# Kernel optimization log

Hardware: AMD Instinct MI355X
Metric: run time of the kernel (lower is better)

The kernel has to match this reference:

```python
import jax, jax.numpy as jnp
import numpy as np

B, V, N = 256, 50, 32
D, H, L, CS, NN, OUT = 128, 384, 12, 10, 10000, 128
ND = N * D          # per-visit input dim
G = 4 * H + 2 * L   # gate projection width
CH = H // L         # chunk size
HS = H // 6         # scale bottleneck


def setup_inputs() -> dict:
    key = jax.random.key(0)
    ks = jax.random.split(key, 20)
    s = 0.02
    embed = jax.random.normal(ks[0], (NN + 1, D), jnp.float32) * s
    embed = embed.at[0].set(0.0)  # padding_idx=0
    inp = {
        'node_ids': jax.random.randint(ks[1], (B, V, N), 0, NN + 1),
        'edge_idx': jax.random.randint(ks[2], (2, 128), 0, NN),
        'edge_attr': jax.random.normal(ks[3], (128,), jnp.float32),
        'time': jax.random.uniform(ks[4], (B, V), jnp.float32),
        'visit_order': jax.random.randint(ks[5], (B, V), 0, V),
        'attn_mask': jnp.ones((B, V), jnp.bool_),
        'embed': embed,
        'kernel_w': jax.random.normal(ks[6], (G, ND + 1), jnp.float32) * s,
        'kernel_b': jnp.zeros((G,), jnp.float32),
        'rec_w': jax.random.normal(ks[7], (G, H + 1), jnp.float32) * s,
        'rec_b': jnp.zeros((G,), jnp.float32),
        'scale_w': jax.random.normal(ks[8], (HS, H), jnp.float32) * s,
        'scale_b': jnp.zeros((HS,), jnp.float32),
        'rescale_w': jax.random.normal(ks[9], (H, HS), jnp.float32) * s,
        'rescale_b': jnp.zeros((H,), jnp.float32),
        'conv_w': jax.random.normal(ks[10], (H, H, CS), jnp.float32) * s,
        'conv_b': jnp.zeros((H,), jnp.float32),
        'out_w': jax.random.normal(ks[11], (OUT, V * H), jnp.float32) * s,
        'out_b': jnp.zeros((OUT,), jnp.float32),
    }
    return inp


def _cumax_l2r(x):
    return jnp.cumsum(jax.nn.softmax(x, -1), -1)


def _cumax_r2l(x):
    return jnp.flip(jnp.cumsum(jax.nn.softmax(jnp.flip(x, -1), -1), -1), -1)


def _forward(node_ids, time, embed, kernel_w, kernel_b, rec_w, rec_b,
             scale_w, scale_b, rescale_w, rescale_b, conv_w, conv_b, out_w, out_b):
    x = embed[node_ids].reshape(B, V, ND)  # gather per-visit code embeddings

    def step(carry, xs):
        c, h, tmp_h, tmp_dis = carry
        x_t, t_t = xs
        iv = t_t[:, None]
        xo = (jnp.concatenate([x_t, iv], -1) @ kernel_w.T + kernel_b
              + jnp.concatenate([h, iv], -1) @ rec_w.T + rec_b)
        fm = _cumax_l2r(xo[:, :L])              # [B,L] master forget
        im = _cumax_r2l(xo[:, L:2 * L])         # [B,L] master input
        g = xo[:, 2 * L:].reshape(B, 4 * L, CH)
        f = jax.nn.sigmoid(g[:, :L])
        i_ = jax.nn.sigmoid(g[:, L:2 * L])
        o = jax.nn.sigmoid(g[:, 2 * L:3 * L])
        cin = jnp.tanh(g[:, 3 * L:])
        cl = c.reshape(B, L, CH)
        fmE, imE = fm[:, :, None], im[:, :, None]
        ov = fmE * imE
        cnew = ov * (f * cl + i_ * cin) + (fmE - ov) * cl + (imE - ov) * cin
        hnew = (o * jnp.tanh(cnew)).reshape(B, H)
        cnew = cnew.reshape(B, H)
        dist = 1.0 - jnp.mean(fm, -1)           # [B]
        tmp_h = jnp.concatenate([tmp_h[1:], hnew[None]], 0)    # [CS,B,H]
        tmp_dis = jnp.concatenate([tmp_dis[1:], dist[None]], 0)  # [CS,B]
        ld = jax.nn.softmax(jnp.cumsum(tmp_dis.T, 1), 1)       # [B,CS]
        lh = tmp_h.transpose(1, 2, 0) * ld[:, None, :]         # [B,H,CS]
        theme = jax.nn.sigmoid(
            jnp.maximum(jnp.mean(lh, -1) @ scale_w.T + scale_b, 0.0)
            @ rescale_w.T + rescale_b)
        conv = jnp.einsum('bhk,ohk->bo', lh, conv_w) + conv_b  # valid conv, len 1
        local = theme * conv
        return (cnew, hnew, tmp_h, tmp_dis), (local, hnew, dist)

    c0 = jnp.zeros((B, H), jnp.float32)
    h0 = jnp.zeros((B, H), jnp.float32)
    tmp_h0 = jnp.zeros((CS, B, H), jnp.float32)
    tmp_dis0 = jnp.zeros((CS, B), jnp.float32)
    xs = (x.transpose(1, 0, 2), time.T)
    _, (hs, ohs, dists) = jax.lax.scan(step, (c0, h0, tmp_h0, tmp_dis0), xs)
    rnn = hs.transpose(1, 0, 2) + ohs.transpose(1, 0, 2)       # [B,V,H]
    out = rnn.reshape(B, V * H) @ out_w.T + out_b
    return out, dists  # dists: [V,B]


def reference(node_ids, edge_idx, edge_attr, time, visit_order, attn_mask,
              embed, kernel_w, kernel_b, rec_w, rec_b, scale_w, scale_b,
              rescale_w, rescale_b, conv_w, conv_b, out_w, out_b):
    # edge_idx / edge_attr / visit_order / attn_mask are unused by StageNet.forward
    return _forward(node_ids, time, embed, kernel_w, kernel_b, rec_w, rec_b,
                    scale_w, scale_b, rescale_w, rescale_b, conv_w, conv_b,
                    out_w, out_b)
```

## Files before the change

kernel.cpp:

```cpp
#include <hip/hip_runtime.h>
#include <math.h>

typedef _Float16 f16;
typedef _Float16 f16x8 __attribute__((ext_vector_type(8)));
typedef float f32x4 __attribute__((ext_vector_type(4)));
typedef unsigned int u32;
typedef u32 u32x4 __attribute__((ext_vector_type(4)));

#define DEV static __device__ __forceinline__

DEV float sigm(float x)  { return 1.0f / (1.0f + __expf(-x)); }
DEV float tanhfast(float x) { return 2.0f / (1.0f + __expf(-2.0f * x)) - 1.0f; }

DEV void gld16(const void* g, void* l) {
  __builtin_amdgcn_global_load_lds((const __attribute__((address_space(1))) void*)g,
                                   (__attribute__((address_space(3))) void*)l, 16, 0, 0);
}

DEV void gbar(int* bar, int nblk) {
  __syncthreads();
  if (threadIdx.x == 0) {
    int* cnt = bar;
    int* gen = bar + 16;
    int g = __hip_atomic_load(gen, __ATOMIC_RELAXED, __HIP_MEMORY_SCOPE_AGENT);
    int a = __hip_atomic_fetch_add(cnt, 1, __ATOMIC_RELEASE, __HIP_MEMORY_SCOPE_AGENT);
    if (a == nblk - 1) {
      __hip_atomic_store(cnt, 0, __ATOMIC_RELAXED, __HIP_MEMORY_SCOPE_AGENT);
      __hip_atomic_store(gen, g + 1, __ATOMIC_RELEASE, __HIP_MEMORY_SCOPE_AGENT);
    } else {
      while (__hip_atomic_load(gen, __ATOMIC_RELAXED, __HIP_MEMORY_SCOPE_AGENT) == g)
        __builtin_amdgcn_s_sleep(1);
    }
    (void)__hip_atomic_load(gen, __ATOMIC_ACQUIRE, __HIP_MEMORY_SCOPE_AGENT);
  }
  __syncthreads();
}

#define GP 1664
#define KH 3840
#define KO 19200
#define ZSPLIT 40
#define NGRP 16
#define NMEM 12
#define NBLK 192
#define XOLS 164
#define RECUR_LDS (122880 + 10496 + 1024)

static constexpr size_t OFF_OPART = 0;
static constexpr size_t OFF_ZB    = 104857600 - 262144;
static constexpr size_t OFF_WK    = 104857600;
static constexpr size_t OFF_XK    = OFF_WK + 13631488;
static constexpr size_t OFF_MLH   = OFF_XK;
static constexpr size_t OFF_S1    = OFF_XK + 9830400;
static constexpr size_t OFF_TH    = OFF_XK + 13107200;
static constexpr size_t OFF_CV    = OFF_XK + 32768000;
static constexpr size_t OFF_SWP   = OFF_XK + 72089600;
static constexpr size_t OFF_RWP2  = OFF_XK + 72187904;
static constexpr size_t OFF_SBP   = OFF_XK + 72286208;
static constexpr size_t OFF_RW    = OFF_XK + 85196800;
static constexpr size_t OFF_SV    = OFF_RW + 1474560;
static constexpr size_t OFF_BAR   = OFF_SV + 8192;
static constexpr size_t OFF_BIASC = OFF_BAR + 32768;
static constexpr size_t OFF_HALL  = OFF_BIASC + 8192;
static constexpr size_t OFF_LD    = OFF_HALL + 9830400;
static constexpr size_t OFF_WC2   = OFF_LD + 512000;
static constexpr size_t OFF_RNN   = OFF_WC2 + 2949120;
static constexpr size_t OFF_OUTW  = OFF_RNN + 9830400;
static constexpr size_t OFF_EH    = OFF_OUTW + 4915200;


__global__ __launch_bounds__(256) void k_prep_wk(const float* __restrict__ kw,
                                                 const float* __restrict__ kb,
                                                 const float* __restrict__ rb,
                                                 f16* __restrict__ Wk,
                                                 float* __restrict__ biasc) {
  long i = (long)blockIdx.x * 256 + threadIdx.x;
  if (i < 1664L * 4096 / 8) {
    long base = i * 8;
    int nn = (int)(base >> 12);
    int k  = (int)(base & 4095);
    f16x8 o;
    if (nn < 1560) {
      const float* s = kw + (long)nn * 4097 + k;
#pragma unroll
      for (int e = 0; e < 8; ++e) o[e] = (f16)s[e];
    } else {
#pragma unroll
      for (int e = 0; e < 8; ++e) o[e] = (f16)0.0f;
    }
    *(f16x8*)(Wk + base) = o;
  }
  if (i < 1664) biasc[i] = (i < 1560) ? (kb[i] + rb[i]) : 0.0f;
}

__global__ __launch_bounds__(512) void k_prep_misc(const float* __restrict__ rw,
                                                   const float* __restrict__ kw,
                                                   const float* __restrict__ sw,
                                                   const float* __restrict__ sb,
                                                   const float* __restrict__ rw2,
                                                   const float* __restrict__ cw,
                                                   const float* __restrict__ ow,
                                                   const float* __restrict__ embed,
                                                   f16* __restrict__ RWp,
                                                   float* __restrict__ Sv,
                                                   int* __restrict__ bar,
                                                   f16* __restrict__ swp,
                                                   float* __restrict__ sbp,
                                                   f16* __restrict__ rwp2,
                                                   f16* __restrict__ Wc2,
                                                   f16* __restrict__ outw,
                                                   f16* __restrict__ Eh) {
  const int blk = blockIdx.x, tid = threadIdx.x;
  if (blk < 180) {
    int i = blk * 512 + tid;
    if (i < 92160) {
      int p = i / 7680;
      int rem = i - p * 7680;
      int tau = rem / 768;
      int r2 = rem - tau * 768;
      int f = r2 >> 6;
      int l = r2 & 63;
      int lc = tau * 16 + (l & 15);
      int n;
      if (lc < 24) n = lc;
      else if (lc < 32) n = -1;
      else { int run = (lc - 32) >> 5; n = 24 + (run * 12 + p) * 32 + ((lc - 32) & 31); }
      int k = f * 32 + ((l >> 4) << 3);
      f16x8 o;
      if (n >= 0) {
        const float* s = rw + (long)n * 385 + k;
#pragma unroll
        for (int e = 0; e < 8; ++e) o[e] = (f16)s[e];
      } else {
#pragma unroll
        for (int e = 0; e < 8; ++e) o[e] = (f16)0.0f;
      }
      *(f16x8*)(RWp + (long)i * 8) = o;
    }
    if (i < 1664)
      Sv[i] = (i < 1560) ? (rw[(long)i * 385 + 384] + kw[(long)i * 4097 + 4096]) : 0.0f;
    if (i < 8192) bar[i] = 0;
  } else if (blk < 276) {
    int i = (blk - 180) * 512 + tid;
    if (i < 128 * 384) {
      int o = i / 384, k = i - o * 384;
      swp[i] = (f16)((o < 64) ? sw[o * 384 + k] : 0.0f);
      int o2 = i >> 7, k2 = i & 127;
      rwp2[i] = (f16)((k2 < 64) ? rw2[o2 * 64 + k2] : 0.0f);
    }
    if (i < 128) sbp[i] = (i < 64) ? sb[i] : 0.0f;
  } else if (blk < 636) {
    int i = (blk - 276) * 512 + tid;
    if (i < 184320) {
      int base = i * 8;
      int o = base / 3840;
      int c = base - o * 3840;
      int j = c / 384;
      int h = c - j * 384;
      f16x8 v;
#pragma unroll
      for (int e = 0; e < 8; ++e) v[e] = (f16)cw[((long)o * 384 + h + e) * 10 + j];
      *(f16x8*)(Wc2 + base) = v;
    }
  } else if (blk < 1236) {
    long i = (long)(blk - 636) * 512 + tid;
    if (i < 307200) {
      long base = i * 8;
      float4 a = *(const float4*)(ow + base);
      float4 b2 = *(const float4*)(ow + base + 4);
      f16x8 v;
      v[0] = (f16)a.x;  v[1] = (f16)a.y;  v[2] = (f16)a.z;  v[3] = (f16)a.w;
      v[4] = (f16)b2.x; v[5] = (f16)b2.y; v[6] = (f16)b2.z; v[7] = (f16)b2.w;
      *(f16x8*)(outw + base) = v;
    }
  } else {
    long i = (long)(blk - 1236) * 512 + tid;
    if (i < 160016) {
      long base = i * 8;
      float4 a = *(const float4*)(embed + base);
      float4 b2 = *(const float4*)(embed + base + 4);
      f16x8 v;
      v[0] = (f16)a.x;  v[1] = (f16)a.y;  v[2] = (f16)a.z;  v[3] = (f16)a.w;
      v[4] = (f16)b2.x; v[5] = (f16)b2.y; v[6] = (f16)b2.z; v[7] = (f16)b2.w;
      *(f16x8*)(Eh + base) = v;
    }
  }
}

__global__ __launch_bounds__(256, 2) void k_gemm_emb(const int* __restrict__ ids,
                                                     const f16* __restrict__ Eh,
                                                     const f16* __restrict__ W,
                                                     f16* __restrict__ C,
                                                     const float* __restrict__ bias) {
  __shared__ __align__(16) f16 As0[256 * 32];
  __shared__ __align__(16) f16 As1[256 * 32];
  __shared__ __align__(16) f16 Bs0[128 * 32];
  __shared__ __align__(16) f16 Bs1[128 * 32];
  const int tid = threadIdx.x;
  const int W0  = blockIdx.y * 50 + blockIdx.x;
  const int xcd = W0 & 7, idx = W0 >> 3;
  const int nw  = (xcd < 2) ? (xcd * 82 + idx) : (164 + (xcd - 2) * 81 + idx);
  const int bx  = nw % 50, by = nw / 50;
  const long rowA0 = (long)bx * 256;
  const long rowB0 = (long)by * 128;
  const int w = tid >> 6, lane = tid & 63;
  const int q = lane >> 4, r16 = lane & 15;
  f32x4 acc[4][8] = {};
  const int srow = tid >> 2;
  const int scol = (tid & 3) * 8;
  const int* idr0 = ids + (rowA0 + srow) * 32;
  const int* idr1 = idr0 + 64 * 32;
  const int* idr2 = idr0 + 128 * 32;
  const int* idr3 = idr0 + 192 * 32;
  const f16* gB0 = W + (rowB0 + srow) * 4096L + scol;
  const f16* gB1 = gB0 + 64L * 4096;
  f16* lA0 = As0 + tid * 8;
  f16* lA1 = As1 + tid * 8;
  f16* lB0 = Bs0 + tid * 8;
  f16* lB1 = Bs1 + tid * 8;
  int cur0 = idr0[0], cur1 = idr1[0], cur2 = idr2[0], cur3 = idr3[0];
  for (int n = 0; n < 32; ++n) {
    int nx0 = 0, nx1 = 0, nx2 = 0, nx3 = 0;
    if (n < 31) { nx0 = idr0[n + 1]; nx1 = idr1[n + 1]; nx2 = idr2[n + 1]; nx3 = idr3[n + 1]; }
#pragma unroll
    for (int kk = 0; kk < 2; ++kk) {
      const int k0 = n * 128 + kk * 64;
      const int d = kk * 64 + scol;
      __syncthreads();
      gld16(Eh + (size_t)cur0 * 128 + d,      lA0);
      gld16(Eh + (size_t)cur1 * 128 + d,      lA0 + 2048);
      gld16(Eh + (size_t)cur2 * 128 + d,      lA0 + 4096);
      gld16(Eh + (size_t)cur3 * 128 + d,      lA0 + 6144);
      gld16(Eh + (size_t)cur0 * 128 + d + 32, lA1);
      gld16(Eh + (size_t)cur1 * 128 + d + 32, lA1 + 2048);
      gld16(Eh + (size_t)cur2 * 128 + d + 32, lA1 + 4096);
      gld16(Eh + (size_t)cur3 * 128 + d + 32, lA1 + 6144);
      gld16(gB0 + k0,      lB0);
      gld16(gB1 + k0,      lB0 + 2048);
      gld16(gB0 + k0 + 32, lB1);
      gld16(gB1 + k0 + 32, lB1 + 2048);
      __syncthreads();
      f16x8 af[4], bf[8];
#pragma unroll
      for (int i = 0; i < 4; i++)
        af[i] = *(const f16x8*)&As0[(w * 64 + i * 16 + r16) * 32 + q * 8];
#pragma unroll
      for (int j = 0; j < 8; j++)
        bf[j] = *(const f16x8*)&Bs0[(j * 16 + r16) * 32 + q * 8];
#pragma unroll
      for (int i = 0; i < 4; i++)
#pragma unroll
        for (int j = 0; j < 8; j++)
          acc[i][j] = __builtin_amdgcn_mfma_f32_16x16x32_f16(af[i], bf[j], acc[i][j], 0, 0, 0);
#pragma unroll
      for (int i = 0; i < 4; i++)
        af[i] = *(const f16x8*)&As1[(w * 64 + i * 16 + r16) * 32 + q * 8];
#pragma unroll
      for (int j = 0; j < 8; j++)
        bf[j] = *(const f16x8*)&Bs1[(j * 16 + r16) * 32 + q * 8];
#pragma unroll
      for (int i = 0; i < 4; i++)
#pragma unroll
        for (int j = 0; j < 8; j++)
          acc[i][j] = __builtin_amdgcn_mfma_f32_16x16x32_f16(af[i], bf[j], acc[i][j], 0, 0, 0);
    }
    cur0 = nx0; cur1 = nx1; cur2 = nx2; cur3 = nx3;
  }
#pragma unroll
  for (int i = 0; i < 4; i++)
#pragma unroll
    for (int j = 0; j < 8; j++) {
      long row = rowA0 + w * 64 + i * 16 + q * 4;
      long col = rowB0 + j * 16 + r16;
      float bv = bias[col];
#pragma unroll
      for (int r = 0; r < 4; r++)
        C[(row + r) * (long)GP + col] = (f16)(acc[i][j][r] + bv);
    }
}

__global__ __launch_bounds__(256) void k_gemm_conv(const float* __restrict__ ld,
                                                   const f16* __restrict__ h_all,
                                                   const f16* __restrict__ W,
                                                   float* __restrict__ C) {
  __shared__ __align__(16) f16 As[128 * 32];
  __shared__ __align__(16) f16 Bs[128 * 32];
  const int tid = threadIdx.x;
  const long rowA0 = (long)blockIdx.x * 128;
  const long rowB0 = (long)blockIdx.y * 128;
  const int ks = blockIdx.z * 1920;
  const long zoff = (long)blockIdx.z * (12800L * 384);
  const int w = tid >> 6, lane = tid & 63;
  const int q = lane >> 4, r16 = lane & 15;
  const int wr = w >> 1, wc = w & 1;
  f32x4 acc[4][4] = {};
  const int srow = tid >> 2;
  const int scol = (tid & 3) * 8;
  const int row0 = (int)rowA0 + srow, row1 = row0 + 64;
  const int b0r = row0 / 50, t0r = row0 - b0r * 50;
  const int b1r = row1 / 50, t1r = row1 - b1r * 50;
  const f16* gB0 = W + (rowB0 + srow) * (long)KH + ks + scol;
  const f16* gB1 = gB0 + 64L * KH;
  f16* lB = Bs + tid * 8;
  for (int k0 = 0; k0 < 1920; k0 += 32) {
    const int col0 = ks + k0;
    const int j = col0 / 384;
    const int hh = col0 - j * 384 + scol;
    const int s0 = t0r - 9 + j, s1 = t1r - 9 + j;
    __syncthreads();
    gld16(gB0 + k0, lB);
    gld16(gB1 + k0, lB + 2048);
    f16x8 a0v = {}, a1v = {};
    if (s0 >= 0) {
      const float lv = ld[row0 * 10 + j];
      f16x8 hv = *(const f16x8*)(h_all + ((size_t)s0 * 256 + b0r) * 384 + hh);
#pragma unroll
      for (int e = 0; e < 8; ++e) a0v[e] = (f16)((float)hv[e] * lv);
    }
    if (s1 >= 0) {
      const float lv = ld[row1 * 10 + j];
      f16x8 hv = *(const f16x8*)(h_all + ((size_t)s1 * 256 + b1r) * 384 + hh);
#pragma unroll
      for (int e = 0; e < 8; ++e) a1v[e] = (f16)((float)hv[e] * lv);
    }
    *(f16x8*)&As[srow * 32 + scol] = a0v;
    *(f16x8*)&As[(srow + 64) * 32 + scol] = a1v;
    __syncthreads();
    f16x8 af[4], bfr[4];
#pragma unroll
    for (int i = 0; i < 4; i++) {
      af[i]  = *(const f16x8*)&As[(wr * 64 + i * 16 + r16) * 32 + q * 8];
      bfr[i] = *(const f16x8*)&Bs[(wc * 64 + i * 16 + r16) * 32 + q * 8];
    }
#pragma unroll
    for (int i = 0; i < 4; i++)
#pragma unroll
      for (int j2 = 0; j2 < 4; j2++)
        acc[i][j2] = __builtin_amdgcn_mfma_f32_16x16x32_f16(af[i], bfr[j2], acc[i][j2], 0, 0, 0);
  }
#pragma unroll
  for (int i = 0; i < 4; i++)
#pragma unroll
    for (int j2 = 0; j2 < 4; j2++) {
      long row = rowA0 + wr * 64 + i * 16 + q * 4;
      long col = rowB0 + wc * 64 + j2 * 16 + r16;
#pragma unroll
      for (int r = 0; r < 4; r++)
        C[(row + r) * 384L + col + zoff] = acc[i][j2][r];
    }
}

__global__ __launch_bounds__(256) void k_gemm_bt(const f16* __restrict__ A,
                                                 const f16* __restrict__ W,
                                                 void* __restrict__ Cv,
                                                 const float* __restrict__ bias,
                                                 int N, int K, int kLen, int act) {
  __shared__ __align__(16) f16 As[128 * 32];
  __shared__ __align__(16) f16 Bs[128 * 32];
  const int tid = threadIdx.x;
  const long rowA0 = (long)blockIdx.x * 128;
  const long rowB0 = (long)blockIdx.y * 128;
  const long ks = (long)blockIdx.z * kLen;
  const long zoff = (long)blockIdx.z * ((long)gridDim.x * 128 * N);
  const int w = tid >> 6, lane = tid & 63;
  const int q = lane >> 4, r16 = lane & 15;
  const int wr = w >> 1, wc = w & 1;
  f32x4 acc[4][4] = {};
  const int srow = tid >> 2;
  const int scol = (tid & 3) * 8;
  const f16* gA0 = A + (rowA0 + srow) * (long)K + ks + scol;
  const f16* gA1 = gA0 + 64L * K;
  const f16* gB0 = W + (rowB0 + srow) * (long)K + ks + scol;
  const f16* gB1 = gB0 + 64L * K;
  f16* lA = As + tid * 8;
  f16* lB = Bs + tid * 8;
  for (int k0 = 0; k0 < kLen; k0 += 32) {
    __syncthreads();
    gld16(gA0 + k0, lA);
    gld16(gA1 + k0, lA + 2048);
    gld16(gB0 + k0, lB);
    gld16(gB1 + k0, lB + 2048);
    __syncthreads();
    f16x8 af[4], bfr[4];
#pragma unroll
    for (int i = 0; i < 4; i++) {
      af[i]  = *(const f16x8*)&As[(wr * 64 + i * 16 + r16) * 32 + q * 8];
      bfr[i] = *(const f16x8*)&Bs[(wc * 64 + i * 16 + r16) * 32 + q * 8];
    }
#pragma unroll
    for (int i = 0; i < 4; i++)
#pragma unroll
      for (int j = 0; j < 4; j++)
        acc[i][j] = __builtin_amdgcn_mfma_f32_16x16x32_f16(af[i], bfr[j], acc[i][j], 0, 0, 0);
  }
#pragma unroll
  for (int i = 0; i < 4; i++)
#pragma unroll
    for (int j = 0; j < 4; j++) {
      long row = rowA0 + wr * 64 + i * 16 + q * 4;
      long col = rowB0 + wc * 64 + j * 16 + r16;
      float bv = bias ? bias[col] : 0.0f;
#pragma unroll
      for (int r = 0; r < 4; r++) {
        float v = acc[i][j][r] + bv;
        long off = (row + r) * (long)N + col + zoff;
        if (act == 0)      ((float*)Cv)[off] = v;
        else if (act == 1) ((f16*)Cv)[off]   = (f16)v;
        else if (act == 2) ((f16*)Cv)[off]   = (f16)fmaxf(v, 0.0f);
        else               ((float*)Cv)[off] = sigm(v);
      }
    }
}

__global__ __launch_bounds__(640)
void k_recur_coop(const f16* __restrict__ XKh,
                  const f16* __restrict__ RWp,
                  const float* __restrict__ Sv,
                  const float* __restrict__ timep,
                  f16* __restrict__ zbuf,
                  f16* __restrict__ hall,
                  float* __restrict__ dists,
                  int* __restrict__ bar) {
  extern __shared__ char smem[];
  f16*   Wl  = (f16*)smem;
  float* xol = (float*)(smem + 122880);
  f16*   hl  = (f16*)(smem + 122880 + 10496);
  const int tid = threadIdx.x;
  const int g = blockIdx.x / NMEM;
  const int m = blockIdx.x - g * NMEM;
  const int b0 = g * 16;
  int* gflags = bar + g * 256;
  int* ibar   = bar + 4096 + g * 32;
  const int w = tid >> 6, lane = tid & 63;
  const int q = lane >> 4, r16 = lane & 15;
  {
    const f16* src = RWp + (size_t)m * 61440;
    for (int i = tid; i < 7680; i += 640)
      *(f16x8*)(Wl + (size_t)i * 8) = *(const f16x8*)(src + (size_t)i * 8);
  }
  int ncol = -1; float Svc = 0.0f;
  if (w < 10) {
    const int lc = w * 16 + r16;
    if (lc < 24) ncol = lc;
    else if (lc >= 32) { int run = (lc - 32) >> 5; ncol = 24 + (run * 12 + m) * 32 + ((lc - 32) & 31); }
    if (ncol >= 0) Svc = Sv[ncol];
  }
  {
    f16x8 z = {};
    for (int i = m * 640 + tid; i < 768; i += NMEM * 640)
      *(f16x8*)(zbuf + (size_t)b0 * 384 + (size_t)i * 8) = z;
  }
  gbar(ibar, NMEM);

  const int ch = tid & 31, bloc = tid >> 5;
  float creg = 0.0f;
  f16 xkc[4] = {};
  if (w < 10 && ncol >= 0) {
#pragma unroll
    for (int r = 0; r < 4; ++r)
      xkc[r] = XKh[((long)(b0 + q * 4 + r) * 50) * GP + ncol];
  }

  for (int t = 0; t < 50; ++t) {
    const f16* hprev = (t == 0) ? zbuf : (hall + (size_t)(t - 1) * 98304);
    f16 xkn[4] = {};
    if (w < 10) {
      f16x8 af[12];
      const f16* ab = hprev + (size_t)(b0 + r16) * 384 + q * 8;
#pragma unroll
      for (int f = 0; f < 12; ++f) af[f] = *(const f16x8*)(ab + f * 32);
      if (t < 49 && ncol >= 0) {
#pragma unroll
        for (int r = 0; r < 4; ++r)
          xkn[r] = XKh[((long)(b0 + q * 4 + r) * 50 + (t + 1)) * GP + ncol];
      }
      float tv4[4];
#pragma unroll
      for (int r = 0; r < 4; ++r) tv4[r] = timep[(b0 + q * 4 + r) * 50 + t];
      const f16* bp = Wl + (size_t)w * 6144 + lane * 8;
      f32x4 a0 = {};
#pragma unroll
      for (int f = 0; f < 12; ++f)
        a0 = __builtin_amdgcn_mfma_f32_16x16x32_f16(af[f], *(const f16x8*)(bp + f * 512), a0, 0, 0, 0);
      const int lc = w * 16 + r16;
#pragma unroll
      for (int r = 0; r < 4; ++r)
        xol[(q * 4 + r) * XOLS + lc] = a0[r] + (float)xkc[r] + tv4[r] * Svc;
    }
    __syncthreads();
    if (bloc < 16) {
      const int gb = b0 + bloc;
      const float* xr = xol + bloc * XOLS;
      float e1[12], e2[12], mx1 = -1e30f, mx2 = -1e30f;
#pragma unroll
      for (int l = 0; l < 12; ++l) {
        e1[l] = xr[l];      mx1 = fmaxf(mx1, e1[l]);
        e2[l] = xr[12 + l]; mx2 = fmaxf(mx2, e2[l]);
      }
      float s1 = 0.0f, s2 = 0.0f;
#pragma unroll
      for (int l = 0; l < 12; ++l) {
        e1[l] = __expf(e1[l] - mx1); s1 += e1[l];
        e2[l] = __expf(e2[l] - mx2); s2 += e2[l];
      }
      float cum1 = 0.0f;
      for (int l = 0; l <= m; ++l) cum1 += e1[l];
      const float fmv = cum1 / s1;
      float cum2 = 0.0f;
      for (int l = 11; l >= m; --l) cum2 += e2[l];
      const float imv = cum2 / s2;
      if (m == 0 && ch == 0) {
        float ds = 0.0f;
#pragma unroll
        for (int l = 0; l < 12; ++l) ds += (float)(12 - l) * e1[l];
        dists[t * 256 + gb] = 1.0f - ds / (12.0f * s1);
      }
      const float fv = sigm(xr[32 + ch]);
      const float iv = sigm(xr[64 + ch]);
      const float og = sigm(xr[96 + ch]);
      const float ci = tanhfast(xr[128 + ch]);
      const float ov = fmv * imv;
      const float cn = ov * (fv * creg + iv * ci) + (fmv - ov) * creg + (imv - ov) * ci;
      creg = cn;
      const float hv = og * tanhfast(cn);
      hl[tid] = (f16)hv;
    }
    __syncthreads();
    if (w == 0) {
      f32x4 d = *(const f32x4*)(hl + lane * 8);
      f16* dst = hall + ((size_t)t * 256 + b0 + (lane >> 2)) * 384 + m * 32 + (lane & 3) * 8;
      asm volatile("global_store_dwordx4 %0, %1, off sc0 sc1\n\t"
                   "s_waitcnt vmcnt(0)"
                   :: "v"(dst), "v"(d) : "memory");
      if (lane == 0) {
        int* fp = gflags + m * 16;
        int fv2 = t + 1;
        asm volatile("global_store_dword %0, %1, off sc0 sc1"
                     :: "v"(fp), "v"(fv2) : "memory");
      }
    }
    if (w == 1 && lane < NMEM) {
      while (__hip_atomic_load(gflags + lane * 16, __ATOMIC_RELAXED, __HIP_MEMORY_SCOPE_AGENT) < t + 1)
        __builtin_amdgcn_s_sleep(1);
    }
    __syncthreads();
    asm volatile("" ::: "memory");
#pragma unroll
    for (int r = 0; r < 4; ++r) xkc[r] = xkn[r];
  }
}

__global__ __launch_bounds__(256) void k_ld(const float* __restrict__ dists,
                                            float* __restrict__ ld) {
  int i = blockIdx.x * 256 + threadIdx.x;
  if (i >= 12800) return;
  int b = i / 50, t = i - b * 50;
  float v[10];
  float cum = 0.0f, mx = -1e30f;
#pragma unroll
  for (int j = 0; j < 10; j++) {
    int s = t - 9 + j;
    float d = (s >= 0) ? dists[s * 256 + b] : 0.0f;
    cum += d; v[j] = cum; mx = fmaxf(mx, cum);
  }
  float sum = 0.0f;
#pragma unroll
  for (int j = 0; j < 10; j++) { v[j] = __expf(v[j] - mx); sum += v[j]; }
  float inv = 1.0f / sum;
#pragma unroll
  for (int j = 0; j < 10; j++) ld[i * 10 + j] = v[j] * inv;
}

__global__ __launch_bounds__(256) void k_mlh(const float* __restrict__ ld,
                                             const f16* __restrict__ h_all,
                                             f16* __restrict__ mlh) {
  int idx = blockIdx.x * 256 + threadIdx.x;
  if (idx >= 614400) return;
  int row = idx / 48, hc = (idx - row * 48) * 8;
  int b = row / 50, t = row - b * 50;
  float acc[8] = {};
#pragma unroll
  for (int j = 0; j < 10; j++) {
    int s = t - 9 + j;
    if (s >= 0) {
      float lv = ld[row * 10 + j];
      f16x8 hv = *(const f16x8*)(h_all + ((size_t)s * 256 + b) * 384 + hc);
#pragma unroll
      for (int e = 0; e < 8; ++e) acc[e] += lv * (float)hv[e];
    }
  }
  f16x8 o;
#pragma unroll
  for (int e = 0; e < 8; ++e) o[e] = (f16)(acc[e] * 0.1f);
  *(f16x8*)(mlh + (size_t)row * 384 + hc) = o;
}

__global__ __launch_bounds__(256) void k_rnn(const float* __restrict__ theme,
                                             const float* __restrict__ convp,
                                             const float* __restrict__ cb,
                                             const f16* __restrict__ h_all,
                                             f16* __restrict__ rnn) {
  int idx = blockIdx.x * 256 + threadIdx.x;
  if (idx >= 614400) return;
  int row = idx / 48, hc = (idx - row * 48) * 8;
  int b = row / 50, t = row - b * 50;
  size_t base = (size_t)row * 384 + hc;
  float4 c0 = *(const float4*)(convp + base);
  float4 c1 = *(const float4*)(convp + base + 4);
  float4 d0 = *(const float4*)(convp + 4915200 + base);
  float4 d1 = *(const float4*)(convp + 4915200 + base + 4);
  float4 t0 = *(const float4*)(theme + base);
  float4 t1 = *(const float4*)(theme + base + 4);
  f16x8 hv = *(const f16x8*)(h_all + ((size_t)t * 256 + b) * 384 + hc);
  f16x8 o;
  o[0] = (f16)(t0.x * (c0.x + d0.x + cb[hc + 0]) + (float)hv[0]);
  o[1] = (f16)(t0.y * (c0.y + d0.y + cb[hc + 1]) + (float)hv[1]);
  o[2] = (f16)(t0.z * (c0.z + d0.z + cb[hc + 2]) + (float)hv[2]);
  o[3] = (f16)(t0.w * (c0.w + d0.w + cb[hc + 3]) + (float)hv[3]);
  o[4] = (f16)(t1.x * (c1.x + d1.x + cb[hc + 4]) + (float)hv[4]);
  o[5] = (f16)(t1.y * (c1.y + d1.y + cb[hc + 5]) + (float)hv[5]);
  o[6] = (f16)(t1.z * (c1.z + d1.z + cb[hc + 6]) + (float)hv[6]);
  o[7] = (f16)(t1.w * (c1.w + d1.w + cb[hc + 7]) + (float)hv[7]);
  *(f16x8*)(rnn + base) = o;
}

__global__ __launch_bounds__(256) void k_red(const float* __restrict__ part,
                                             const float* __restrict__ ob,
                                             float* __restrict__ out) {
  int i = blockIdx.x * 256 + threadIdx.x;
  float s = 0.0f;
#pragma unroll
  for (int z = 0; z < ZSPLIT; z++) s += part[z * 32768 + i];
  out[i] = s + ob[i & 127];
}

extern "C" void kernel_launch(void* const* d_in, const int* in_sizes, int n_in,
                              void* d_out, int out_size, void* d_ws, size_t ws_size,
                              hipStream_t stream) {
  (void)in_sizes; (void)n_in; (void)out_size; (void)ws_size;
  const int*   node_ids  = (const int*)  d_in[0];
  const float* timep     = (const float*)d_in[3];
  const float* embed     = (const float*)d_in[6];
  const float* kernel_w  = (const float*)d_in[7];
  const float* kernel_b  = (const float*)d_in[8];
  const float* rec_w     = (const float*)d_in[9];
  const float* rec_b     = (const float*)d_in[10];
  const float* scale_w   = (const float*)d_in[11];
  const float* scale_b   = (const float*)d_in[12];
  const float* rescale_w = (const float*)d_in[13];
  const float* rescale_b = (const float*)d_in[14];
  const float* conv_w    = (const float*)d_in[15];
  const float* conv_b    = (const float*)d_in[16];
  const float* out_w     = (const float*)d_in[17];
  const float* out_b     = (const float*)d_in[18];

  char* ws = (char*)d_ws;
  float* opart   = (float*)(ws + OFF_OPART);
  f16*   zbuf    = (f16*)  (ws + OFF_ZB);
  f16*   Wk      = (f16*)  (ws + OFF_WK);
  f16*   XKh     = (f16*)  (ws + OFF_XK);
  f16*   mlh_h   = (f16*)  (ws + OFF_MLH);
  f16*   s1h     = (f16*)  (ws + OFF_S1);
  float* theme   = (float*)(ws + OFF_TH);
  float* convbuf = (float*)(ws + OFF_CV);
  f16*   swp     = (f16*)  (ws + OFF_SWP);
  f16*   rwp2    = (f16*)  (ws + OFF_RWP2);
  float* sbp     = (float*)(ws + OFF_SBP);
  f16*   RWp     = (f16*)  (ws + OFF_RW);
  float* Sv      = (float*)(ws + OFF_SV);
  int*   bar     = (int*)  (ws + OFF_BAR);
  float* biasc   = (float*)(ws + OFF_BIASC);
  f16*   h_all   = (f16*)  (ws + OFF_HALL);
  float* ldbuf   = (float*)(ws + OFF_LD);
  f16*   Wc2     = (f16*)  (ws + OFF_WC2);
  f16*   rnn     = (f16*)  (ws + OFF_RNN);
  f16*   outw    = (f16*)  (ws + OFF_OUTW);
  f16*   Eh      = (f16*)  (ws + OFF_EH);

  float* outp  = (float*)d_out;
  float* dists = outp + 256 * 128;

  k_prep_wk  <<<3332, 256, 0, stream>>>(kernel_w, kernel_b, rec_b, Wk, biasc);
  k_prep_misc<<<1549, 512, 0, stream>>>(rec_w, kernel_w, scale_w, scale_b, rescale_w,
                                        conv_w, out_w, embed,
                                        RWp, Sv, bar, swp, sbp, rwp2, Wc2, outw, Eh);
  k_gemm_emb<<<dim3(50, 13), 256, 0, stream>>>(node_ids, Eh, Wk, XKh, biasc);
  {
    hipFuncSetAttribute((const void*)k_recur_coop,
                        hipFuncAttributeMaxDynamicSharedMemorySize, RECUR_LDS);
    void* cargs[] = {(void*)&XKh, (void*)&RWp, (void*)&Sv, (void*)&timep,
                     (void*)&zbuf, (void*)&h_all, (void*)&dists, (void*)&bar};
    hipLaunchCooperativeKernel((void*)k_recur_coop, dim3(NBLK), dim3(640),
                               cargs, RECUR_LDS, stream);
  }
  k_ld  <<<50,   256, 0, stream>>>(dists, ldbuf);
  k_mlh <<<2400, 256, 0, stream>>>(ldbuf, h_all, mlh_h);
  k_gemm_bt<<<dim3(100, 1), 256, 0, stream>>>(mlh_h, swp, s1h, sbp, 128, 384, 384, 2);
  k_gemm_bt<<<dim3(100, 3), 256, 0, stream>>>(s1h, rwp2, theme, rescale_b, 384, 128, 128, 3);
  k_gemm_conv<<<dim3(100, 3, 2), 256, 0, stream>>>(ldbuf, h_all, Wc2, convbuf);
  k_rnn <<<2400, 256, 0, stream>>>(theme, convbuf, conv_b, h_all, rnn);
  k_gemm_bt<<<dim3(2, 1, ZSPLIT), 256, 0, stream>>>(rnn, outw, opart, nullptr, 128, KO, KO / ZSPLIT, 0);
  k_red<<<128, 256, 0, stream>>>(opart, out_b, outp);
}
```

Before: 893.0 us.

## Double-buffer gathered GEMM tiles to overlap global loads with MFMA

Restructures the embedding-gather GEMM main loop into a software pipeline over 128 K-steps of 32. The next step's A (gathered embedding rows) and B tiles are issued into the alternate LDS buffer while MFMAs run on the current buffer, with one barrier per step instead of two. The aim is to hide global-load latency behind compute. The cost is finer-grained steps with more barriers per unit of work, and it depends on the async LDS loads being waited on correctly at the barrier.

```diff
diff --git a/kernel.cpp b/kernel.cpp
--- a/kernel.cpp
+++ b/kernel.cpp
@@ -214,57 +214,57 @@
   const int* idr3 = idr0 + 192 * 32;
   const f16* gB0 = W + (rowB0 + srow) * 4096L + scol;
   const f16* gB1 = gB0 + 64L * 4096;
-  f16* lA0 = As0 + tid * 8;
-  f16* lA1 = As1 + tid * 8;
-  f16* lB0 = Bs0 + tid * 8;
-  f16* lB1 = Bs1 + tid * 8;
   int cur0 = idr0[0], cur1 = idr1[0], cur2 = idr2[0], cur3 = idr3[0];
-  for (int n = 0; n < 32; ++n) {
-    int nx0 = 0, nx1 = 0, nx2 = 0, nx3 = 0;
-    if (n < 31) { nx0 = idr0[n + 1]; nx1 = idr1[n + 1]; nx2 = idr2[n + 1]; nx3 = idr3[n + 1]; }
-#pragma unroll
-    for (int kk = 0; kk < 2; ++kk) {
-      const int k0 = n * 128 + kk * 64;
-      const int d = kk * 64 + scol;
-      __syncthreads();
-      gld16(Eh + (size_t)cur0 * 128 + d,      lA0);
-      gld16(Eh + (size_t)cur1 * 128 + d,      lA0 + 2048);
-      gld16(Eh + (size_t)cur2 * 128 + d,      lA0 + 4096);
-      gld16(Eh + (size_t)cur3 * 128 + d,      lA0 + 6144);
-      gld16(Eh + (size_t)cur0 * 128 + d + 32, lA1);
-      gld16(Eh + (size_t)cur1 * 128 + d + 32, lA1 + 2048);
-      gld16(Eh + (size_t)cur2 * 128 + d + 32, lA1 + 4096);
-      gld16(Eh + (size_t)cur3 * 128 + d + 32, lA1 + 6144);
-      gld16(gB0 + k0,      lB0);
-      gld16(gB1 + k0,      lB0 + 2048);
-      gld16(gB0 + k0 + 32, lB1);
-      gld16(gB1 + k0 + 32, lB1 + 2048);
-      __syncthreads();
+  int nx0 = idr0[1], nx1 = idr1[1], nx2 = idr2[1], nx3 = idr3[1];
+
+  {
+    gld16(Eh + (size_t)cur0 * 128 + scol, As0 + tid * 8);
+    gld16(Eh + (size_t)cur1 * 128 + scol, As0 + tid * 8 + 2048);
+    gld16(Eh + (size_t)cur2 * 128 + scol, As0 + tid * 8 + 4096);
+    gld16(Eh + (size_t)cur3 * 128 + scol, As0 + tid * 8 + 6144);
+    gld16(gB0, Bs0 + tid * 8);
+    gld16(gB1, Bs0 + tid * 8 + 2048);
+  }
+  __syncthreads();
+
+#pragma unroll 2
+  for (int s = 0; s < 128; ++s) {
+    if (s < 127) {
+      const int sn = s + 1;
+      if ((sn & 3) == 0) {
+        cur0 = nx0; cur1 = nx1; cur2 = nx2; cur3 = nx3;
+        const int gg = (sn >> 2) + 1;
+        if (gg < 32) { nx0 = idr0[gg]; nx1 = idr1[gg]; nx2 = idr2[gg]; nx3 = idr3[gg]; }
+      }
+      const int n = sn >> 2, kk = sn & 3;
+      const int d = kk * 32 + scol;
+      const int k0 = n * 128 + kk * 32;
+      f16* lA = ((sn & 1) ? As1 : As0) + tid * 8;
+      f16* lB = ((sn & 1) ? Bs1 : Bs0) + tid * 8;
+      gld16(Eh + (size_t)cur0 * 128 + d, lA);
+      gld16(Eh + (size_t)cur1 * 128 + d, lA + 2048);
+      gld16(Eh + (size_t)cur2 * 128 + d, lA + 4096);
+      gld16(Eh + (size_t)cur3 * 128 + d, lA + 6144);
+      gld16(gB0 + k0, lB);
+      gld16(gB1 + k0, lB + 2048);
+    }
+    {
+      const f16* Ab = (s & 1) ? As1 : As0;
+      const f16* Bb = (s & 1) ? Bs1 : Bs0;
       f16x8 af[4], bf[8];
 #pragma unroll
       for (int i = 0; i < 4; i++)
-        af[i] = *(const f16x8*)&As0[(w * 64 + i * 16 + r16) * 32 + q * 8];
+        af[i] = *(const f16x8*)&Ab[(w * 64 + i * 16 + r16) * 32 + q * 8];
 #pragma unroll
       for (int j = 0; j < 8; j++)
-        bf[j] = *(const f16x8*)&Bs0[(j * 16 + r16) * 32 + q * 8];
+        bf[j] = *(const f16x8*)&Bb[(j * 16 + r16) * 32 + q * 8];
 #pragma unroll
       for (int i = 0; i < 4; i++)
 #pragma unroll
         for (int j = 0; j < 8; j++)
           acc[i][j] = __builtin_amdgcn_mfma_f32_16x16x32_f16(af[i], bf[j], acc[i][j], 0, 0, 0);
-#pragma unroll
-      for (int i = 0; i < 4; i++)
-        af[i] = *(const f16x8*)&As1[(w * 64 + i * 16 + r16) * 32 + q * 8];
-#pragma unroll
-      for (int j = 0; j < 8; j++)
-        bf[j] = *(const f16x8*)&Bs1[(j * 16 + r16) * 32 + q * 8];
-#pragma unroll
-      for (int i = 0; i < 4; i++)
-#pragma unroll
-        for (int j = 0; j < 8; j++)
-          acc[i][j] = __builtin_amdgcn_mfma_f32_16x16x32_f16(af[i], bf[j], acc[i][j], 0, 0, 0);
-    }
-    cur0 = nx0; cur1 = nx1; cur2 = nx2; cur3 = nx3;
+    }
+    __syncthreads();
   }
 #pragma unroll
   for (int i = 0; i < 4; i++)
```

Result: slower. 924.8 us (+3.6%).

## Fuse rnn epilogue into conv GEMM and drop split-K partial buffer

Applied to the files above, without the earlier changes.

The conv GEMM now covers the full K range (no split-K over two z slices) with 64-row tiles, and applies the conv bias, theme multiply and h residual directly in its epilogue to write the f16 rnn output. The separate k_rnn kernel and the fp32 conv partial buffers are removed. This saves a launch and the write and re-read of two fp32 12800x384 partial arrays plus the theme read pass. In exchange each block runs a loop twice as long with smaller tiles and lower MFMA reuse, and the epilogue does scattered scalar loads and stores.

```diff
diff --git a/kernel.cpp b/kernel.cpp
--- a/kernel.cpp
+++ b/kernel.cpp
@@ -282,72 +282,63 @@
 __global__ __launch_bounds__(256) void k_gemm_conv(const float* __restrict__ ld,
                                                    const f16* __restrict__ h_all,
                                                    const f16* __restrict__ W,
-                                                   float* __restrict__ C) {
-  __shared__ __align__(16) f16 As[128 * 32];
+                                                   const float* __restrict__ theme,
+                                                   const float* __restrict__ cb,
+                                                   f16* __restrict__ rnn) {
+  __shared__ __align__(16) f16 As[64 * 32];
   __shared__ __align__(16) f16 Bs[128 * 32];
   const int tid = threadIdx.x;
-  const long rowA0 = (long)blockIdx.x * 128;
-  const long rowB0 = (long)blockIdx.y * 128;
-  const int ks = blockIdx.z * 1920;
-  const long zoff = (long)blockIdx.z * (12800L * 384);
+  const int rowA0 = blockIdx.x * 64;
+  const int rowB0 = blockIdx.y * 128;
   const int w = tid >> 6, lane = tid & 63;
   const int q = lane >> 4, r16 = lane & 15;
-  const int wr = w >> 1, wc = w & 1;
-  f32x4 acc[4][4] = {};
+  f32x4 acc[8] = {};
   const int srow = tid >> 2;
   const int scol = (tid & 3) * 8;
-  const int row0 = (int)rowA0 + srow, row1 = row0 + 64;
+  const int row0 = rowA0 + srow;
   const int b0r = row0 / 50, t0r = row0 - b0r * 50;
-  const int b1r = row1 / 50, t1r = row1 - b1r * 50;
-  const f16* gB0 = W + (rowB0 + srow) * (long)KH + ks + scol;
+  const f16* gB0 = W + (rowB0 + srow) * (long)KH + scol;
   const f16* gB1 = gB0 + 64L * KH;
   f16* lB = Bs + tid * 8;
-  for (int k0 = 0; k0 < 1920; k0 += 32) {
-    const int col0 = ks + k0;
-    const int j = col0 / 384;
-    const int hh = col0 - j * 384 + scol;
-    const int s0 = t0r - 9 + j, s1 = t1r - 9 + j;
+  for (int k0 = 0; k0 < 3840; k0 += 32) {
+    const int j = k0 / 384;
+    const int hh = k0 - j * 384 + scol;
+    const int s0 = t0r - 9 + j;
     __syncthreads();
     gld16(gB0 + k0, lB);
     gld16(gB1 + k0, lB + 2048);
-    f16x8 a0v = {}, a1v = {};
+    f16x8 a0v = {};
     if (s0 >= 0) {
       const float lv = ld[row0 * 10 + j];
       f16x8 hv = *(const f16x8*)(h_all + ((size_t)s0 * 256 + b0r) * 384 + hh);
 #pragma unroll
       for (int e = 0; e < 8; ++e) a0v[e] = (f16)((float)hv[e] * lv);
     }
-    if (s1 >= 0) {
-      const float lv = ld[row1 * 10 + j];
-      f16x8 hv = *(const f16x8*)(h_all + ((size_t)s1 * 256 + b1r) * 384 + hh);
-#pragma unroll
-      for (int e = 0; e < 8; ++e) a1v[e] = (f16)((float)hv[e] * lv);
-    }
     *(f16x8*)&As[srow * 32 + scol] = a0v;
-    *(f16x8*)&As[(srow + 64) * 32 + scol] = a1v;
     __syncthreads();
-    f16x8 af[4], bfr[4];
-#pragma unroll
-    for (int i = 0; i < 4; i++) {
-      af[i]  = *(const f16x8*)&As[(wr * 64 + i * 16 + r16) * 32 + q * 8];
-      bfr[i] = *(const f16x8*)&Bs[(wc * 64 + i * 16 + r16) * 32 + q * 8];
-    }
-#pragma unroll
-    for (int i = 0; i < 4; i++)
-#pragma unroll
-      for (int j2 = 0; j2 < 4; j2++)
-        acc[i][j2] = __builtin_amdgcn_mfma_f32_16x16x32_f16(af[i], bfr[j2], acc[i][j2], 0, 0, 0);
-  }
-#pragma unroll
-  for (int i = 0; i < 4; i++)
-#pragma unroll
-    for (int j2 = 0; j2 < 4; j2++) {
-      long row = rowA0 + wr * 64 + i * 16 + q * 4;
-      long col = rowB0 + wc * 64 + j2 * 16 + r16;
-#pragma unroll
-      for (int r = 0; r < 4; r++)
-        C[(row + r) * 384L + col + zoff] = acc[i][j2][r];
-    }
+    f16x8 af = *(const f16x8*)&As[(w * 16 + r16) * 32 + q * 8];
+    f16x8 bf[8];
+#pragma unroll
+    for (int j2 = 0; j2 < 8; j2++)
+      bf[j2] = *(const f16x8*)&Bs[(j2 * 16 + r16) * 32 + q * 8];
+#pragma unroll
+    for (int j2 = 0; j2 < 8; j2++)
+      acc[j2] = __builtin_amdgcn_mfma_f32_16x16x32_f16(af, bf[j2], acc[j2], 0, 0, 0);
+  }
+#pragma unroll
+  for (int j2 = 0; j2 < 8; j2++) {
+    const int col = rowB0 + j2 * 16 + r16;
+    const float cbv = cb[col];
+#pragma unroll
+    for (int r = 0; r < 4; r++) {
+      const int rw = rowA0 + w * 16 + q * 4 + r;
+      const int b = rw / 50, t = rw - b * 50;
+      const float v = acc[j2][r] + cbv;
+      const float th = theme[(size_t)rw * 384 + col];
+      const float hvv = (float)h_all[((size_t)t * 256 + b) * 384 + col];
+      rnn[(size_t)rw * 384 + col] = (f16)(th * v + hvv);
+    }
+  }
 }
 
 __global__ __launch_bounds__(256) void k_gemm_bt(const f16* __restrict__ A,
@@ -595,35 +586,6 @@
   *(f16x8*)(mlh + (size_t)row * 384 + hc) = o;
 }
 
-__global__ __launch_bounds__(256) void k_rnn(const float* __restrict__ theme,
-                                             const float* __restrict__ convp,
-                                             const float* __restrict__ cb,
-                                             const f16* __restrict__ h_all,
-                                             f16* __restrict__ rnn) {
-  int idx = blockIdx.x * 256 + threadIdx.x;
-  if (idx >= 614400) return;
-  int row = idx / 48, hc = (idx - row * 48) * 8;
-  int b = row / 50, t = row - b * 50;
-  size_t base = (size_t)row * 384 + hc;
-  float4 c0 = *(const float4*)(convp + base);
-  float4 c1 = *(const float4*)(convp + base + 4);
-  float4 d0 = *(const float4*)(convp + 4915200 + base);
-  float4 d1 = *(const float4*)(convp + 4915200 + base + 4);
-  float4 t0 = *(const float4*)(theme + base);
-  float4 t1 = *(const float4*)(theme + base + 4);
-  f16x8 hv = *(const f16x8*)(h_all + ((size_t)t * 256 + b) * 384 + hc);
-  f16x8 o;
-  o[0] = (f16)(t0.x * (c0.x + d0.x + cb[hc + 0]) + (float)hv[0]);
-  o[1] = (f16)(t0.y * (c0.y + d0.y + cb[hc + 1]) + (float)hv[1]);
-  o[2] = (f16)(t0.z * (c0.z + d0.z + cb[hc + 2]) + (float)hv[2]);
-  o[3] = (f16)(t0.w * (c0.w + d0.w + cb[hc + 3]) + (float)hv[3]);
-  o[4] = (f16)(t1.x * (c1.x + d1.x + cb[hc + 4]) + (float)hv[4]);
-  o[5] = (f16)(t1.y * (c1.y + d1.y + cb[hc + 5]) + (float)hv[5]);
-  o[6] = (f16)(t1.z * (c1.z + d1.z + cb[hc + 6]) + (float)hv[6]);
-  o[7] = (f16)(t1.w * (c1.w + d1.w + cb[hc + 7]) + (float)hv[7]);
-  *(f16x8*)(rnn + base) = o;
-}
-
 __global__ __launch_bounds__(256) void k_red(const float* __restrict__ part,
                                              const float* __restrict__ ob,
                                              float* __restrict__ out) {
@@ -662,7 +624,6 @@
   f16*   mlh_h   = (f16*)  (ws + OFF_MLH);
   f16*   s1h     = (f16*)  (ws + OFF_S1);
   float* theme   = (float*)(ws + OFF_TH);
-  float* convbuf = (float*)(ws + OFF_CV);
   f16*   swp     = (f16*)  (ws + OFF_SWP);
   f16*   rwp2    = (f16*)  (ws + OFF_RWP2);
   float* sbp     = (float*)(ws + OFF_SBP);
@@ -697,8 +658,7 @@
   k_mlh <<<2400, 256, 0, stream>>>(ldbuf, h_all, mlh_h);
   k_gemm_bt<<<dim3(100, 1), 256, 0, stream>>>(mlh_h, swp, s1h, sbp, 128, 384, 384, 2);
   k_gemm_bt<<<dim3(100, 3), 256, 0, stream>>>(s1h, rwp2, theme, rescale_b, 384, 128, 128, 3);
-  k_gemm_conv<<<dim3(100, 3, 2), 256, 0, stream>>>(ldbuf, h_all, Wc2, convbuf);
-  k_rnn <<<2400, 256, 0, stream>>>(theme, convbuf, conv_b, h_all, rnn);
+  k_gemm_conv<<<dim3(200, 3), 256, 0, stream>>>(ldbuf, h_all, Wc2, theme, conv_b, rnn);
   k_gemm_bt<<<dim3(2, 1, ZSPLIT), 256, 0, stream>>>(rnn, outw, opart, nullptr, 128, KO, KO / ZSPLIT, 0);
   k_red<<<128, 256, 0, stream>>>(opart, out_b, outp);
 }
```

After: 906.2 us. About the same (+1.5%).
